# Optimization experiments

Hardware: AMD Instinct MI355X
Metric: run time of the kernel (lower is better)

## Reference

```python
import math
import jax, jax.numpy as jnp
import numpy as np

N_STEPS = 4

def rotate_half(x):
    h = x.shape[-1] // 2
    return jnp.concatenate([-x[..., h:], x[..., :h]], axis=-1)

def setup_inputs() -> dict:
    key = jax.random.key(0)
    k0, k1, k2, k3 = jax.random.split(key, 4)
    B, N, F, D = 2, 4096, 512, 64
    features = jax.random.normal(k0, (B, N, F), jnp.float32)
    # standard RoPE tables, shape [N, D]
    inv_freq = 1.0 / (10000.0 ** (jnp.arange(0, D, 2, dtype=jnp.float32) / D))
    ang = jnp.arange(N, dtype=jnp.float32)[:, None] * inv_freq[None, :]  # [N, D/2]
    ang = jnp.concatenate([ang, ang], axis=-1)  # [N, D]
    cos, sin = jnp.cos(ang), jnp.sin(ang)
    # causal mask broadcast to [B, N, N]
    mask = jnp.broadcast_to(jnp.tril(jnp.ones((N, N), bool)), (B, N, N))
    s = 1.0 / math.sqrt(F)
    Wq = jax.random.normal(k1, (F, D), jnp.float32) * s
    Wk = jax.random.normal(k2, (F, D), jnp.float32) * s
    charge_w = jax.random.normal(k3, (F, 1), jnp.float32) * s
    charge_b = jnp.zeros((1,), jnp.float32)
    step_size = jnp.full((1,), 0.5, jnp.float32)
    charge_decay = jnp.full((1,), 0.3, jnp.float32)
    return dict(features=features, cos=cos, sin=sin, mask=mask, Wq=Wq, Wk=Wk,
                charge_w=charge_w, charge_b=charge_b,
                step_size=step_size, charge_decay=charge_decay)

def reference(features, cos, sin, mask, Wq, Wk, charge_w, charge_b, step_size, charge_decay):
    d_k = Wq.shape[-1]
    Q = jnp.einsum('bnf,fd->bnd', features, Wq)
    K = jnp.einsum('bnf,fd->bnd', features, Wk)
    c, s = cos[None, :, :], sin[None, :, :]  # broadcast over batch
    Q = Q * c + rotate_half(Q) * s
    K = K * c + rotate_half(K) * s
    compat = jnp.einsum('bnd,bmd->bnm', Q, K) / math.sqrt(d_k)  # [B,N,N]
    charge = jax.nn.sigmoid(jnp.einsum('bnf,fo->bno', features, charge_w)[..., 0] + charge_b[0])  # [B,N]
    neg_inf = jnp.asarray(-jnp.inf, compat.dtype)
    logits = jnp.where(mask, compat, neg_inf)
    ss = step_size[0]
    cd = charge_decay[0]
    for _ in range(N_STEPS):
        attn = jax.nn.softmax(logits, axis=-1)
        received = attn.sum(axis=-2)  # column sums, [B,N]
        charge = charge * (1.0 - cd * jax.nn.sigmoid(received - 1.0))
        energy = -compat * charge[..., :, None] * charge[..., None, :]
        logits = jnp.where(mask, logits - ss * energy, neg_inf)
    return jax.nn.softmax(logits, axis=-1)
```

## Files before the change

kernel.cpp:

```cpp
#include <hip/hip_runtime.h>
#include <math.h>

#define NTOK   4096
#define NFEAT  512
#define NDIM   64
#define RROWS  8
#define NBANDS 512

__global__ __launch_bounds__(256) void qk_kernel(
    const float* __restrict__ feat, const float* __restrict__ cosb,
    const float* __restrict__ sinb, const float* __restrict__ Wq,
    const float* __restrict__ Wk, const float* __restrict__ cw,
    const float* __restrict__ cbp, float* __restrict__ Q, float* __restrict__ K,
    float* __restrict__ cur)
{
  __shared__ __align__(16) float smem[RROWS * NFEAT];
  const int tid  = threadIdx.x;
  const int row0 = blockIdx.x * RROWS;

  const float4* fb4 = (const float4*)(feat + (size_t)row0 * NFEAT);
  float4* sm4 = (float4*)smem;
#pragma unroll
  for (int i = tid; i < RROWS * NFEAT / 4; i += 256) sm4[i] = fb4[i];
  __syncthreads();

  const int r   = tid >> 5;
  const int c   = tid & 31;
  const int isQ = (c < 16);
  const int d0  = (c & 15) * 4;
  const float* __restrict__ Wp = isQ ? Wq : Wk;
  const float* fr = smem + (r << 9);

  float a0 = 0.f, a1 = 0.f, a2 = 0.f, a3 = 0.f;
  for (int k = 0; k < NFEAT; ++k) {
    float fv = fr[k];
    float4 w = *(const float4*)(Wp + k * NDIM + d0);
    a0 = fmaf(fv, w.x, a0); a1 = fmaf(fv, w.y, a1);
    a2 = fmaf(fv, w.z, a2); a3 = fmaf(fv, w.w, a3);
  }

  float accc = 0.f;
#pragma unroll
  for (int j = 0; j < 16; ++j) accc = fmaf(fr[c + (j << 5)], cw[c + (j << 5)], accc);
#pragma unroll
  for (int o = 16; o > 0; o >>= 1) accc += __shfl_down(accc, o, 64);
  if (c == 0) {
    float cb = cbp[0];
    cur[row0 + r] = 1.f / (1.f + __expf(-(accc + cb)));
  }
  __syncthreads();

  float* sraw = smem;
  {
    float* dst = sraw + r * 132 + (isQ ? 0 : 64) + d0;
    dst[0] = a0; dst[1] = a1; dst[2] = a2; dst[3] = a3;
  }
  __syncthreads();

#pragma unroll
  for (int i = tid; i < RROWS * NDIM; i += 256) {
    int rr = i >> 6, d = i & 63;
    int g = row0 + rr, n = g & (NTOK - 1);
    float cv = cosb[(n << 6) + d], sv = sinb[(n << 6) + d];
    float qv = sraw[rr * 132 + d];
    float qr = (d < 32) ? -sraw[rr * 132 + d + 32] : sraw[rr * 132 + d - 32];
    Q[(size_t)g * NDIM + d] = qv * cv + qr * sv;
    float kv = sraw[rr * 132 + 64 + d];
    float kr = (d < 32) ? -sraw[rr * 132 + 64 + d + 32] : sraw[rr * 132 + 64 + d - 32];
    K[(size_t)g * NDIM + d] = kv * cv + kr * sv;
  }
}

__global__ __launch_bounds__(256) void compat_kernel(
    const float* __restrict__ Q, const float* __restrict__ K, float* __restrict__ C)
{
  __shared__ __align__(16) float Qs[32][132];
  __shared__ __align__(16) float Ks[32][132];
  int p = blockIdx.x, b = 0;
  if (p >= 528) { b = 1; p -= 528; }
  int ti = (int)((sqrtf(8.f * p + 1.f) - 1.f) * 0.5f);
  while ((ti + 1) * (ti + 2) / 2 <= p) ++ti;
  while (ti * (ti + 1) / 2 > p) --ti;
  int tj = p - ti * (ti + 1) / 2;

  const int tid = threadIdx.x;
  const int ty = tid >> 4, tx = tid & 15;
  const int i0 = ty * 8, j0 = tx * 8;
  const size_t qbase = ((size_t)b * NTOK + (size_t)ti * 128) * NDIM;
  const size_t kbase = ((size_t)b * NTOK + (size_t)tj * 128) * NDIM;

  float acc[8][8];
#pragma unroll
  for (int ii = 0; ii < 8; ++ii)
#pragma unroll
    for (int jj = 0; jj < 8; ++jj) acc[ii][jj] = 0.f;

  for (int dk = 0; dk < NDIM; dk += 32) {
    __syncthreads();
    for (int i = tid; i < 128 * 32; i += 256) {
      int row = i >> 5, d = i & 31;
      Qs[d][row] = Q[qbase + (size_t)row * NDIM + dk + d];
      Ks[d][row] = K[kbase + (size_t)row * NDIM + dk + d];
    }
    __syncthreads();
#pragma unroll
    for (int d = 0; d < 32; ++d) {
      float4 q0 = *(const float4*)&Qs[d][i0];
      float4 q1 = *(const float4*)&Qs[d][i0 + 4];
      float4 k0 = *(const float4*)&Ks[d][j0];
      float4 k1 = *(const float4*)&Ks[d][j0 + 4];
      float av[8] = {q0.x, q0.y, q0.z, q0.w, q1.x, q1.y, q1.z, q1.w};
      float bv[8] = {k0.x, k0.y, k0.z, k0.w, k1.x, k1.y, k1.z, k1.w};
#pragma unroll
      for (int ii = 0; ii < 8; ++ii)
#pragma unroll
        for (int jj = 0; jj < 8; ++jj)
          acc[ii][jj] = fmaf(av[ii], bv[jj], acc[ii][jj]);
    }
  }
#pragma unroll
  for (int ii = 0; ii < 8; ++ii) {
    size_t grow = (size_t)b * NTOK + (size_t)ti * 128 + i0 + ii;
    float4 w0 = make_float4(acc[ii][0] * 0.125f, acc[ii][1] * 0.125f,
                            acc[ii][2] * 0.125f, acc[ii][3] * 0.125f);
    float4 w1 = make_float4(acc[ii][4] * 0.125f, acc[ii][5] * 0.125f,
                            acc[ii][6] * 0.125f, acc[ii][7] * 0.125f);
    *(float4*)&C[grow * NTOK + (size_t)tj * 128 + j0]     = w0;
    *(float4*)&C[grow * NTOK + (size_t)tj * 128 + j0 + 4] = w1;
  }
}

template <int MODE, int NC>
__global__ __launch_bounds__(256) void pass_kernel(
    const float* __restrict__ compat, const float* __restrict__ chistT,
    const float* __restrict__ ssp, float* __restrict__ partial,
    float* __restrict__ out)
{
  __shared__ float rp[NTOK];
  const int tid = threadIdx.x;
  int p = blockIdx.x, b = 0;
  if (p >= NBANDS) { b = 1; p -= NBANDS; }
  const int w = __builtin_amdgcn_readfirstlane(tid >> 6);
  const int l = tid & 63;
  const float ss = ssp[0];
  const float* __restrict__ chT = chistT + (b << 12);

  if (MODE == 0) {
    for (int i = tid; i < NTOK; i += 256) rp[i] = 0.f;
    __syncthreads();
  }

  for (int half = 0; half < 2; ++half) {
    const int n = half ? (NTOK - 1 - ((p << 2) + w)) : ((p << 2) + w);
    const int scmax = n >> 8;
    const float4* __restrict__ rowv =
        (const float4*)(compat + ((size_t)((b << 12) + n) << 12));
    float h[NC > 0 ? NC : 1];
#pragma unroll
    for (int c = 0; c < NC; ++c) h[c] = ss * chT[(c << 13) + n];

    float4 ev[16];
#pragma unroll
    for (int sc = 0; sc < 16; ++sc)
      ev[sc] = make_float4(-INFINITY, -INFINITY, -INFINITY, -INFINITY);

    float vmax = -INFINITY;
#pragma unroll
    for (int ph = 0; ph < 4; ++ph) {
      if ((ph << 10) > n) continue;
      float4 cv[4];
#pragma unroll
      for (int j = 0; j < 4; ++j)
        cv[j] = rowv[(((ph << 2) + j) << 6) + l];
#pragma unroll
      for (int j = 0; j < 4; ++j) {
        const int sc = (ph << 2) + j;
        if ((sc << 8) > n) continue;
        const int base = (sc << 8) + (l << 2);
        float4 dot = make_float4(0.f, 0.f, 0.f, 0.f);
#pragma unroll
        for (int c = 0; c < NC; ++c) {
          float4 g = *(const float4*)(chT + (c << 13) + base);
          dot.x = fmaf(g.x, h[c], dot.x);
          dot.y = fmaf(g.y, h[c], dot.y);
          dot.z = fmaf(g.z, h[c], dot.z);
          dot.w = fmaf(g.w, h[c], dot.w);
        }
        float4 q = cv[j], x;
        x.x = fmaf(q.x, dot.x, q.x);
        x.y = fmaf(q.y, dot.y, q.y);
        x.z = fmaf(q.z, dot.z, q.z);
        x.w = fmaf(q.w, dot.w, q.w);
        x.x = (base + 0 <= n) ? x.x : -INFINITY;
        x.y = (base + 1 <= n) ? x.y : -INFINITY;
        x.z = (base + 2 <= n) ? x.z : -INFINITY;
        x.w = (base + 3 <= n) ? x.w : -INFINITY;
        ev[sc] = x;
        vmax = fmaxf(vmax, fmaxf(fmaxf(x.x, x.y), fmaxf(x.z, x.w)));
      }
    }
#pragma unroll
    for (int o = 32; o > 0; o >>= 1) vmax = fmaxf(vmax, __shfl_xor(vmax, o, 64));

    float s = 0.f;
#pragma unroll
    for (int sc = 0; sc < 16; ++sc) {
      if (sc > scmax) continue;
      float4 v;
      v.x = __expf(ev[sc].x - vmax);
      v.y = __expf(ev[sc].y - vmax);
      v.z = __expf(ev[sc].z - vmax);
      v.w = __expf(ev[sc].w - vmax);
      ev[sc] = v;
      s += (v.x + v.y) + (v.z + v.w);
    }
#pragma unroll
    for (int o = 32; o > 0; o >>= 1) s += __shfl_xor(s, o, 64);
    const float inv = 1.f / s;

    if (MODE == 0) {
#pragma unroll
      for (int sc = 0; sc < 16; ++sc) {
        if (sc > scmax) continue;
        const int slot = (sc << 8) + l;
        atomicAdd(&rp[slot      ], ev[sc].x * inv);
        atomicAdd(&rp[slot +  64], ev[sc].y * inv);
        atomicAdd(&rp[slot + 128], ev[sc].z * inv);
        atomicAdd(&rp[slot + 192], ev[sc].w * inv);
      }
    } else {
      float4* __restrict__ orow =
          (float4*)(out + ((size_t)((b << 12) + n) << 12));
#pragma unroll
      for (int sc = 0; sc < 16; ++sc) {
        if (sc > scmax) continue;
        float4 v = ev[sc];
        v.x *= inv; v.y *= inv; v.z *= inv; v.w *= inv;
        orow[(sc << 6) + l] = v;
      }
    }
  }

  if (MODE == 0) {
    __syncthreads();
    float4* __restrict__ pp4 =
        (float4*)(partial + ((size_t)b * NBANDS + p) * (size_t)NTOK);
    const float4* rp4 = (const float4*)rp;
    for (int i = tid; i < NTOK / 4; i += 256) pp4[i] = rp4[i];
  }
}

__global__ __launch_bounds__(256) void reduce_update_kernel(
    const float* __restrict__ partial, const float* __restrict__ cdp,
    float* __restrict__ cur, float* __restrict__ chistT, int step)
{
  __shared__ float s[8][32];
  const int tid = threadIdx.x;
  const int b = blockIdx.x >> 7;
  const int s0 = (blockIdx.x & 127) << 5;
  const int ml = tid & 31, seg = tid >> 5;
  const int slot = s0 + ml;
  const int m = (slot & ~255) | ((slot & 63) << 2) | ((slot >> 6) & 3);
  int pmax = (NTOK - 1 - m) >> 2;
  if (pmax > NBANDS - 1) pmax = NBANDS - 1;
  float sum = 0.f;
  const float* pb = partial + (size_t)b * NBANDS * NTOK + slot;
  for (int band = seg; band <= pmax; band += 8)
    sum += pb[(size_t)band << 12];
  s[seg][ml] = sum;
  __syncthreads();
  if (seg == 0) {
    float r = s[0][ml] + s[1][ml] + s[2][ml] + s[3][ml] +
              s[4][ml] + s[5][ml] + s[6][ml] + s[7][ml];
    float sg = 1.f / (1.f + __expf(-(r - 1.f)));
    float cd = cdp[0];
    int idx = (b << 12) + m;
    float c = cur[idx] * (1.f - cd * sg);
    cur[idx] = c;
    chistT[(step << 13) + idx] = c;
  }
}

extern "C" void kernel_launch(void* const* d_in, const int* in_sizes, int n_in,
                              void* d_out, int out_size, void* d_ws, size_t ws_size,
                              hipStream_t stream) {
  const float* feat = (const float*)d_in[0];
  const float* cosb = (const float*)d_in[1];
  const float* sinb = (const float*)d_in[2];
  const float* Wq  = (const float*)d_in[4];
  const float* Wk  = (const float*)d_in[5];
  const float* cw  = (const float*)d_in[6];
  const float* cbp = (const float*)d_in[7];
  const float* ssp = (const float*)d_in[8];
  const float* cdp = (const float*)d_in[9];
  float* out = (float*)d_out;

  float* ws      = (float*)d_ws;
  float* Q       = ws;
  float* K       = ws + 524288;
  float* chistT  = ws + 1048576;
  float* cur     = ws + 1081344;
  float* partial = ws + 1089536;

  qk_kernel<<<1024, 256, 0, stream>>>(feat, cosb, sinb, Wq, Wk, cw, cbp, Q, K, cur);
  compat_kernel<<<1056, 256, 0, stream>>>(Q, K, out);

  pass_kernel<0, 0><<<2 * NBANDS, 256, 0, stream>>>(out, chistT, ssp, partial, nullptr);
  reduce_update_kernel<<<256, 256, 0, stream>>>(partial, cdp, cur, chistT, 0);
  pass_kernel<0, 1><<<2 * NBANDS, 256, 0, stream>>>(out, chistT, ssp, partial, nullptr);
  reduce_update_kernel<<<256, 256, 0, stream>>>(partial, cdp, cur, chistT, 1);
  pass_kernel<0, 2><<<2 * NBANDS, 256, 0, stream>>>(out, chistT, ssp, partial, nullptr);
  reduce_update_kernel<<<256, 256, 0, stream>>>(partial, cdp, cur, chistT, 2);
  pass_kernel<0, 3><<<2 * NBANDS, 256, 0, stream>>>(out, chistT, ssp, partial, nullptr);
  reduce_update_kernel<<<256, 256, 0, stream>>>(partial, cdp, cur, chistT, 3);
  pass_kernel<1, 4><<<2 * NBANDS, 256, 0, stream>>>(out, chistT, ssp, nullptr, out);
}
```

Before: 823.5 us.

## Restructure softmax pass to 8 contiguous rows per block with load-all-first

The pass kernel now uses 512-thread blocks that each handle 8 consecutive rows, one per wave. Bands are launched in reverse order so the long rows start first. Each row loads all of its compat chunks up front, either 16 or 8 chunks depending on the row range, with a scheduling barrier so the loads are issued together. This replaces the earlier scheme that paired a short row with a long row for balance and used phased loads. The column-sum reduction is updated to match the new band-to-row mapping. The change aims for more memory-level parallelism and fewer per-lane branches, at the cost of more registers per thread and work that is less even across blocks.

```diff
diff --git a/kernel.cpp b/kernel.cpp
--- a/kernel.cpp
+++ b/kernel.cpp
@@ -130,123 +130,122 @@
   }
 }
 
+template <int MODE, int NSC, int NC>
+__device__ __forceinline__ void row_body(
+    const int b, const int n, const int l,
+    const float* __restrict__ compat, const float* __restrict__ chT,
+    const float ss, float* __restrict__ rp, float* __restrict__ out)
+{
+  const int scmax = n >> 8;
+  const float4* __restrict__ rowv =
+      (const float4*)(compat + ((size_t)((b << 12) + n) << 12));
+
+  float4 cv[NSC];
+#pragma unroll
+  for (int sc = 0; sc < NSC; ++sc) cv[sc] = rowv[(sc << 6) + l];
+  __builtin_amdgcn_sched_barrier(0);
+
+  float h[NC > 0 ? NC : 1];
+#pragma unroll
+  for (int c = 0; c < NC; ++c) h[c] = ss * chT[(c << 13) + n];
+
+  float vmax = -INFINITY;
+#pragma unroll
+  for (int sc = 0; sc < NSC; ++sc) {
+    const int base = (sc << 8) + (l << 2);
+    float dx = 0.f, dy = 0.f, dz = 0.f, dw = 0.f;
+#pragma unroll
+    for (int c = 0; c < NC; ++c) {
+      float4 g = *(const float4*)(chT + (c << 13) + base);
+      dx = fmaf(g.x, h[c], dx);
+      dy = fmaf(g.y, h[c], dy);
+      dz = fmaf(g.z, h[c], dz);
+      dw = fmaf(g.w, h[c], dw);
+    }
+    float4 q = cv[sc], x;
+    x.x = fmaf(q.x, dx, q.x);
+    x.y = fmaf(q.y, dy, q.y);
+    x.z = fmaf(q.z, dz, q.z);
+    x.w = fmaf(q.w, dw, q.w);
+    x.x = (base + 0 <= n) ? x.x : -INFINITY;
+    x.y = (base + 1 <= n) ? x.y : -INFINITY;
+    x.z = (base + 2 <= n) ? x.z : -INFINITY;
+    x.w = (base + 3 <= n) ? x.w : -INFINITY;
+    cv[sc] = x;
+    vmax = fmaxf(vmax, fmaxf(fmaxf(x.x, x.y), fmaxf(x.z, x.w)));
+  }
+#pragma unroll
+  for (int o = 32; o > 0; o >>= 1) vmax = fmaxf(vmax, __shfl_xor(vmax, o, 64));
+
+  float ssum = 0.f;
+#pragma unroll
+  for (int sc = 0; sc < NSC; ++sc) {
+    float4 v;
+    v.x = __expf(cv[sc].x - vmax);
+    v.y = __expf(cv[sc].y - vmax);
+    v.z = __expf(cv[sc].z - vmax);
+    v.w = __expf(cv[sc].w - vmax);
+    cv[sc] = v;
+    ssum += (v.x + v.y) + (v.z + v.w);
+  }
+#pragma unroll
+  for (int o = 32; o > 0; o >>= 1) ssum += __shfl_xor(ssum, o, 64);
+  const float inv = 1.f / ssum;
+
+  if (MODE == 0) {
+#pragma unroll
+    for (int sc = 0; sc < NSC; ++sc) {
+      if (sc > scmax) continue;
+      const int slot = (sc << 8) + l;
+      atomicAdd(&rp[slot      ], cv[sc].x * inv);
+      atomicAdd(&rp[slot +  64], cv[sc].y * inv);
+      atomicAdd(&rp[slot + 128], cv[sc].z * inv);
+      atomicAdd(&rp[slot + 192], cv[sc].w * inv);
+    }
+  } else {
+    float4* __restrict__ orow = (float4*)(out + ((size_t)((b << 12) + n) << 12));
+#pragma unroll
+    for (int sc = 0; sc < NSC; ++sc) {
+      if (sc > scmax) continue;
+      float4 v = cv[sc];
+      v.x *= inv; v.y *= inv; v.z *= inv; v.w *= inv;
+      orow[(sc << 6) + l] = v;
+    }
+  }
+}
+
 template <int MODE, int NC>
-__global__ __launch_bounds__(256) void pass_kernel(
+__global__ __launch_bounds__(512) void pass_kernel(
     const float* __restrict__ compat, const float* __restrict__ chistT,
     const float* __restrict__ ssp, float* __restrict__ partial,
     float* __restrict__ out)
 {
   __shared__ float rp[NTOK];
   const int tid = threadIdx.x;
-  int p = blockIdx.x, b = 0;
-  if (p >= NBANDS) { b = 1; p -= NBANDS; }
+  const int b    = blockIdx.x >> 9;
+  const int band = (NBANDS - 1) - (blockIdx.x & (NBANDS - 1));
   const int w = __builtin_amdgcn_readfirstlane(tid >> 6);
   const int l = tid & 63;
+  const int n = (band << 3) + w;
   const float ss = ssp[0];
   const float* __restrict__ chT = chistT + (b << 12);
 
   if (MODE == 0) {
-    for (int i = tid; i < NTOK; i += 256) rp[i] = 0.f;
+    for (int i = tid; i < NTOK; i += 512) rp[i] = 0.f;
     __syncthreads();
   }
 
-  for (int half = 0; half < 2; ++half) {
-    const int n = half ? (NTOK - 1 - ((p << 2) + w)) : ((p << 2) + w);
-    const int scmax = n >> 8;
-    const float4* __restrict__ rowv =
-        (const float4*)(compat + ((size_t)((b << 12) + n) << 12));
-    float h[NC > 0 ? NC : 1];
-#pragma unroll
-    for (int c = 0; c < NC; ++c) h[c] = ss * chT[(c << 13) + n];
-
-    float4 ev[16];
-#pragma unroll
-    for (int sc = 0; sc < 16; ++sc)
-      ev[sc] = make_float4(-INFINITY, -INFINITY, -INFINITY, -INFINITY);
-
-    float vmax = -INFINITY;
-#pragma unroll
-    for (int ph = 0; ph < 4; ++ph) {
-      if ((ph << 10) > n) continue;
-      float4 cv[4];
-#pragma unroll
-      for (int j = 0; j < 4; ++j)
-        cv[j] = rowv[(((ph << 2) + j) << 6) + l];
-#pragma unroll
-      for (int j = 0; j < 4; ++j) {
-        const int sc = (ph << 2) + j;
-        if ((sc << 8) > n) continue;
-        const int base = (sc << 8) + (l << 2);
-        float4 dot = make_float4(0.f, 0.f, 0.f, 0.f);
-#pragma unroll
-        for (int c = 0; c < NC; ++c) {
-          float4 g = *(const float4*)(chT + (c << 13) + base);
-          dot.x = fmaf(g.x, h[c], dot.x);
-          dot.y = fmaf(g.y, h[c], dot.y);
-          dot.z = fmaf(g.z, h[c], dot.z);
-          dot.w = fmaf(g.w, h[c], dot.w);
-        }
-        float4 q = cv[j], x;
-        x.x = fmaf(q.x, dot.x, q.x);
-        x.y = fmaf(q.y, dot.y, q.y);
-        x.z = fmaf(q.z, dot.z, q.z);
-        x.w = fmaf(q.w, dot.w, q.w);
-        x.x = (base + 0 <= n) ? x.x : -INFINITY;
-        x.y = (base + 1 <= n) ? x.y : -INFINITY;
-        x.z = (base + 2 <= n) ? x.z : -INFINITY;
-        x.w = (base + 3 <= n) ? x.w : -INFINITY;
-        ev[sc] = x;
-        vmax = fmaxf(vmax, fmaxf(fmaxf(x.x, x.y), fmaxf(x.z, x.w)));
-      }
-    }
-#pragma unroll
-    for (int o = 32; o > 0; o >>= 1) vmax = fmaxf(vmax, __shfl_xor(vmax, o, 64));
-
-    float s = 0.f;
-#pragma unroll
-    for (int sc = 0; sc < 16; ++sc) {
-      if (sc > scmax) continue;
-      float4 v;
-      v.x = __expf(ev[sc].x - vmax);
-      v.y = __expf(ev[sc].y - vmax);
-      v.z = __expf(ev[sc].z - vmax);
-      v.w = __expf(ev[sc].w - vmax);
-      ev[sc] = v;
-      s += (v.x + v.y) + (v.z + v.w);
-    }
-#pragma unroll
-    for (int o = 32; o > 0; o >>= 1) s += __shfl_xor(s, o, 64);
-    const float inv = 1.f / s;
-
-    if (MODE == 0) {
-#pragma unroll
-      for (int sc = 0; sc < 16; ++sc) {
-        if (sc > scmax) continue;
-        const int slot = (sc << 8) + l;
-        atomicAdd(&rp[slot      ], ev[sc].x * inv);
-        atomicAdd(&rp[slot +  64], ev[sc].y * inv);
-        atomicAdd(&rp[slot + 128], ev[sc].z * inv);
-        atomicAdd(&rp[slot + 192], ev[sc].w * inv);
-      }
-    } else {
-      float4* __restrict__ orow =
-          (float4*)(out + ((size_t)((b << 12) + n) << 12));
-#pragma unroll
-      for (int sc = 0; sc < 16; ++sc) {
-        if (sc > scmax) continue;
-        float4 v = ev[sc];
-        v.x *= inv; v.y *= inv; v.z *= inv; v.w *= inv;
-        orow[(sc << 6) + l] = v;
-      }
-    }
-  }
+  if (band >= 256)
+    row_body<MODE, 16, NC>(b, n, l, compat, chT, ss, rp, out);
+  else
+    row_body<MODE, 8, NC>(b, n, l, compat, chT, ss, rp, out);
 
   if (MODE == 0) {
     __syncthreads();
     float4* __restrict__ pp4 =
-        (float4*)(partial + ((size_t)b * NBANDS + p) * (size_t)NTOK);
+        (float4*)(partial + ((size_t)b * NBANDS + band) * (size_t)NTOK);
     const float4* rp4 = (const float4*)rp;
-    for (int i = tid; i < NTOK / 4; i += 256) pp4[i] = rp4[i];
+    for (int i = tid; i < NTOK / 4; i += 512) pp4[i] = rp4[i];
   }
 }
 
@@ -261,11 +260,10 @@
   const int ml = tid & 31, seg = tid >> 5;
   const int slot = s0 + ml;
   const int m = (slot & ~255) | ((slot & 63) << 2) | ((slot >> 6) & 3);
-  int pmax = (NTOK - 1 - m) >> 2;
-  if (pmax > NBANDS - 1) pmax = NBANDS - 1;
+  const int bmin = m >> 3;
   float sum = 0.f;
   const float* pb = partial + (size_t)b * NBANDS * NTOK + slot;
-  for (int band = seg; band <= pmax; band += 8)
+  for (int band = bmin + seg; band < NBANDS; band += 8)
     sum += pb[(size_t)band << 12];
   s[seg][ml] = sum;
   __syncthreads();
@@ -305,13 +303,13 @@
   qk_kernel<<<1024, 256, 0, stream>>>(feat, cosb, sinb, Wq, Wk, cw, cbp, Q, K, cur);
   compat_kernel<<<1056, 256, 0, stream>>>(Q, K, out);
 
-  pass_kernel<0, 0><<<2 * NBANDS, 256, 0, stream>>>(out, chistT, ssp, partial, nullptr);
+  pass_kernel<0, 0><<<1024, 512, 0, stream>>>(out, chistT, ssp, partial, nullptr);
   reduce_update_kernel<<<256, 256, 0, stream>>>(partial, cdp, cur, chistT, 0);
-  pass_kernel<0, 1><<<2 * NBANDS, 256, 0, stream>>>(out, chistT, ssp, partial, nullptr);
+  pass_kernel<0, 1><<<1024, 512, 0, stream>>>(out, chistT, ssp, partial, nullptr);
   reduce_update_kernel<<<256, 256, 0, stream>>>(partial, cdp, cur, chistT, 1);
-  pass_kernel<0, 2><<<2 * NBANDS, 256, 0, stream>>>(out, chistT, ssp, partial, nullptr);
+  pass_kernel<0, 2><<<1024, 512, 0, stream>>>(out, chistT, ssp, partial, nullptr);
   reduce_update_kernel<<<256, 256, 0, stream>>>(partial, cdp, cur, chistT, 2);
-  pass_kernel<0, 3><<<2 * NBANDS, 256, 0, stream>>>(out, chistT, ssp, partial, nullptr);
+  pass_kernel<0, 3><<<1024, 512, 0, stream>>>(out, chistT, ssp, partial, nullptr);
   reduce_update_kernel<<<256, 256, 0, stream>>>(partial, cdp, cur, chistT, 3);
-  pass_kernel<1, 4><<<2 * NBANDS, 256, 0, stream>>>(out, chistT, ssp, nullptr, out);
-}
+  pass_kernel<1, 4><<<1024, 512, 0, stream>>>(out, chistT, ssp, nullptr, out);
+}
```

Measured after the change: 923.9 us. +12.2%, slower.
